# Optimization experiments

Measured on AMD Instinct MI355X. Metric: run time of the kernel, lower is better.

Reference implementation:

```python
import jax, jax.numpy as jnp
import numpy as np
from jax import lax

NEG_INF = -jnp.inf

def _conv_same(x, w, b):
    # x: [B,C,H,W], w: [O,C,5,5], padding=2 (SAME for k=5)
    y = lax.conv_general_dilated(x, w, (1, 1), [(2, 2), (2, 2)],
                                 dimension_numbers=('NCHW', 'OIHW', 'NCHW'))
    return y + b[None, :, None, None]

def _maxpool3(x):
    # kernel=3, stride=3, VALID: 28x28 -> 9x9
    return lax.reduce_window(x, -jnp.inf, lax.max, (1, 1, 3, 3), (1, 1, 3, 3), 'VALID')

def _trunk(x, w1, b1, w2, b2):
    # x: [B,1,28,28] -> [B, 16*9*9]
    h = jax.nn.relu(_conv_same(x, w1, b1))
    h = jax.nn.relu(_conv_same(h, w2, b2))
    h = _maxpool3(h)
    return h.reshape(h.shape[0], -1)

def _iterator(state, c_w1, c_b1, c_w2, c_b2, c_wl, c_bl):
    # state: [B,28,28]
    B = state.shape[0]
    xd = state[:, None]                                   # [B,1,28,28]
    feat = _trunk(xd, c_w1, c_b1, c_w2, c_b2)             # [B,1296]
    w = jnp.tanh(feat @ c_wl + c_bl).reshape(B, 1, 13, 13)  # per-sample kernels [O=B,I=1,13,13]
    xp = jnp.pad(xd, ((0, 0), (0, 0), (6, 6), (6, 6)), constant_values=-1.0)  # [B,1,40,40]
    xg = xp.reshape(1, B, 40, 40)
    yg = lax.conv_general_dilated(xg, w, (1, 1), 'VALID',
                                  feature_group_count=B,
                                  dimension_numbers=('NCHW', 'OIHW', 'NCHW'))  # [1,B,28,28]
    return yg.reshape(B, 28, 28)

def setup_inputs() -> dict:
    key = jax.random.key(0)
    ks = jax.random.split(key, 13)
    s = 0.05
    B = 1024
    inp = {
        'x': jax.random.normal(ks[0], (B, 28, 28), jnp.float32),
        # determine_n params
        'n_w1': jax.random.normal(ks[1], (8, 1, 5, 5), jnp.float32) * s,
        'n_b1': jnp.zeros((8,), jnp.float32),
        'n_w2': jax.random.normal(ks[2], (16, 8, 5, 5), jnp.float32) * s,
        'n_b2': jnp.zeros((16,), jnp.float32),
        'n_wl': jax.random.normal(ks[3], (16 * 9 * 9, 10), jnp.float32) * s,
        'n_bl': jnp.zeros((10,), jnp.float32),
        # determine_conv params
        'c_w1': jax.random.normal(ks[4], (8, 1, 5, 5), jnp.float32) * s,
        'c_b1': jnp.zeros((8,), jnp.float32),
        'c_w2': jax.random.normal(ks[5], (16, 8, 5, 5), jnp.float32) * s,
        'c_b2': jnp.zeros((16,), jnp.float32),
        'c_wl': jax.random.normal(ks[6], (16 * 9 * 9, 13 * 13), jnp.float32) * s,
        'c_bl': jnp.zeros((13 * 13,), jnp.float32),
    }
    return inp

def reference(x, n_w1, n_b1, n_w2, n_b2, n_wl, n_bl,
              c_w1, c_b1, c_w2, c_b2, c_wl, c_bl):
    B = x.shape[0]
    xd = x.reshape(B, 1, 28, 28)
    # determine_n: soft natural number over {0..9}
    num = jnp.tanh(_trunk(xd, n_w1, n_b1, n_w2, n_b2) @ n_wl + n_bl)  # [B,10]
    # TmIter: weighted sum of iterates r_0..r_9, r_{k+1} = iterator(r_k)
    r = x
    out = num[:, 0, None, None] * r
    for k in range(1, 10):  # fixed 9-step unroll (num encodes naturals 0..9)
        r = _iterator(r, c_w1, c_b1, c_w2, c_b2, c_wl, c_bl)
        out = out + num[:, k, None, None] * r
    return out.reshape(-1, 28, 28)
```

## Files before the change

kernel.cpp:

```cpp
#include <hip/hip_runtime.h>
#include <math.h>

#define RP40S 44
#define H1W   31

struct SharedBufs {
    float rp40[2][40*RP40S];
    float h1p[8*28*H1W];
    float pbuf[1296];
    float wker[13*16];
    float num_s[10];
    int   next;
};

template<int OUT, bool PAD>
__device__ __forceinline__ void fc_tanh(const float* __restrict__ Wg,
                                        const float* __restrict__ bg,
                                        const float* __restrict__ p,
                                        float* __restrict__ dst, int tid)
{
    if (tid < OUT) {
        float a[8];
        #pragma unroll
        for (int u = 0; u < 8; ++u) a[u] = 0.f;
        #pragma unroll 8
        for (int i0 = 0; i0 < 1296; i0 += 8) {
            const float4 p0 = *(const float4*)&p[i0];
            const float4 p1 = *(const float4*)&p[i0+4];
            a[0] = fmaf(p0.x, Wg[(i0+0)*OUT + tid], a[0]);
            a[1] = fmaf(p0.y, Wg[(i0+1)*OUT + tid], a[1]);
            a[2] = fmaf(p0.z, Wg[(i0+2)*OUT + tid], a[2]);
            a[3] = fmaf(p0.w, Wg[(i0+3)*OUT + tid], a[3]);
            a[4] = fmaf(p1.x, Wg[(i0+4)*OUT + tid], a[4]);
            a[5] = fmaf(p1.y, Wg[(i0+5)*OUT + tid], a[5]);
            a[6] = fmaf(p1.z, Wg[(i0+6)*OUT + tid], a[6]);
            a[7] = fmaf(p1.w, Wg[(i0+7)*OUT + tid], a[7]);
        }
        float s = ((a[0]+a[1])+(a[2]+a[3])) + ((a[4]+a[5])+(a[6]+a[7])) + bg[tid];
        dst[PAD ? (tid/13)*16 + (tid%13) : tid] = tanhf(s);
    }
}

__device__ __forceinline__ void conv1_corr(const float* __restrict__ w1g,
                                           const float* __restrict__ b1g,
                                           int c, int y,
                                           float& base, float& e0, float& e1,
                                           float& e26, float& e27)
{
    float wreg[25];
    #pragma unroll
    for (int t = 0; t < 25; ++t) wreg[t] = w1g[c*25 + t];
    float csR[5];
    float S_all = 0.f, SR = 0.f;
    #pragma unroll
    for (int kx = 0; kx < 5; ++kx) {
        float a = wreg[kx] + wreg[5+kx] + wreg[10+kx] + wreg[15+kx] + wreg[20+kx];
        float ex = 0.f;
        if (y == 0)       ex = wreg[kx] + wreg[5+kx];
        else if (y == 1)  ex = wreg[kx];
        if (y == 26)      ex += wreg[20+kx];
        else if (y == 27) ex += wreg[15+kx] + wreg[20+kx];
        csR[kx] = a - ex;
        S_all += a; SR += csR[kx];
    }
    base = b1g[c] + (S_all - SR);
    e0  = csR[0] + csR[1];
    e1  = csR[0];
    e26 = csR[4];
    e27 = csR[3] + csR[4];
}

#define C2_LOADROW(dst, YY) {                                                  \
    int rr_ = crow0 + (YY); rr_ = rr_ < 2 ? 2 : (rr_ > 29 ? 29 : rr_);         \
    const float* hp_ = plane + (rr_ - 2)*H1W;                                  \
    _Pragma("unroll") for (int j = 0; j < 13; ++j) dst[j] = hp_[j]; }

#define C2_FMAROW(src, YY)                                                     \
    if ((unsigned)(crow0 + (YY) - 2) <= 27u) {                                 \
      _Pragma("unroll") for (int t = 0; t < 3; ++t) {                          \
        const int ky_ = (YY) - t;                                              \
        if (ky_ >= 0 && ky_ <= 4) {                                            \
          _Pragma("unroll") for (int kx = 0; kx < 5; ++kx) {                   \
            const float w_ = wreg[ky_*5+kx];                                   \
            _Pragma("unroll") for (int u = 0; u < 9; ++u)                      \
              acc[t*9+u] = fmaf(w_, src[u+kx], acc[t*9+u]); } } } }

__device__ __forceinline__ void trunk_pass(SharedBufs& sb,
                                           const float* __restrict__ rpc,
                                           int tid,
                                           const float* __restrict__ w1g,
                                           const float* __restrict__ w2g,
                                           const float* __restrict__ b2g,
                                           float base, float e0, float e1,
                                           float e26, float e27)
{
    if (tid < 224) {
        const int c = tid & 7;
        const int y = tid >> 3;
        float wreg[25];
        #pragma unroll
        for (int t = 0; t < 25; ++t) wreg[t] = w1g[c*25 + t];
        float acc[28];
        #pragma unroll
        for (int x = 0; x < 28; ++x) acc[x] = base;
        acc[0]  += e0;
        acc[1]  += e1;
        acc[26] += e26;
        acc[27] += e27;
        #pragma unroll
        for (int ky = 0; ky < 5; ++ky) {
            const float4* rr = (const float4*)&rpc[(y+4+ky)*RP40S + 4];
            float rv[32];
            #pragma unroll
            for (int q = 0; q < 8; ++q) {
                float4 t = rr[q];
                rv[q*4+0]=t.x; rv[q*4+1]=t.y; rv[q*4+2]=t.z; rv[q*4+3]=t.w;
            }
            #pragma unroll
            for (int kx = 0; kx < 5; ++kx) {
                const float w = wreg[ky*5+kx];
                #pragma unroll
                for (int x = 0; x < 28; ++x) acc[x] = fmaf(w, rv[x+kx], acc[x]);
            }
        }
        float* hp = &sb.h1p[(c*28 + y)*H1W + 2];
        #pragma unroll
        for (int x = 0; x < 28; ++x) hp[x] = fmaxf(acc[x], 0.f);
    }
    __syncthreads();

    if (tid < 240) {
        const int c    = tid / 15;
        const int rem  = tid % 15;
        const int pyg  = rem / 3;
        const int pxg  = rem % 3;
        const int col0 = pxg * 9;
        const float bias = b2g[c];
        #pragma unroll 1
        for (int h = 0; h < 2; ++h) {
            const int py = pyg*2 + h;
            if (py >= 9) break;
            const int crow0 = py * 3;
            float acc[27];
            #pragma unroll
            for (int i = 0; i < 27; ++i) acc[i] = bias;
            for (int ic = 0; ic < 8; ++ic) {
                float wreg[25];
                const float* wsrc = &w2g[(c*8+ic)*25];
                #pragma unroll
                for (int t = 0; t < 25; ++t) wreg[t] = wsrc[t];
                const float* plane = &sb.h1p[ic*28*H1W + col0];
                float ra[13], rb[13];
                C2_LOADROW(ra, 0)
                C2_LOADROW(rb, 1)  C2_FMAROW(ra, 0)
                C2_LOADROW(ra, 2)  C2_FMAROW(rb, 1)
                C2_LOADROW(rb, 3)  C2_FMAROW(ra, 2)
                C2_LOADROW(ra, 4)  C2_FMAROW(rb, 3)
                C2_LOADROW(rb, 5)  C2_FMAROW(ra, 4)
                C2_LOADROW(ra, 6)  C2_FMAROW(rb, 5)
                                   C2_FMAROW(ra, 6)
            }
            #pragma unroll
            for (int pxi = 0; pxi < 3; ++pxi) {
                float m = acc[pxi*3];
                #pragma unroll
                for (int dy = 0; dy < 3; ++dy)
                    #pragma unroll
                    for (int dx = 0; dx < 3; ++dx)
                        m = fmaxf(m, acc[dy*9 + pxi*3 + dx]);
                sb.pbuf[c*81 + py*9 + pxg*3 + pxi] = fmaxf(m, 0.f);
            }
        }
    }
    __syncthreads();
}

__device__ __forceinline__ void depthwise13_regs(SharedBufs& sb,
                                                 const float* __restrict__ rpc,
                                                 int y, int x0,
                                                 float& a0, float& a1,
                                                 float& a2, float& a3)
{
    a0=0.f; a1=0.f; a2=0.f; a3=0.f;
    #pragma unroll 1
    for (int ky = 0; ky < 13; ++ky) {
        const float4* rr = (const float4*)&rpc[(y+ky)*RP40S + x0];
        float rv[16];
        #pragma unroll
        for (int q = 0; q < 4; ++q) {
            float4 t = rr[q];
            rv[q*4+0]=t.x; rv[q*4+1]=t.y; rv[q*4+2]=t.z; rv[q*4+3]=t.w;
        }
        const float4* wq = (const float4*)&sb.wker[ky*16];
        float wv[16];
        #pragma unroll
        for (int q = 0; q < 4; ++q) {
            float4 t = wq[q];
            wv[q*4+0]=t.x; wv[q*4+1]=t.y; wv[q*4+2]=t.z; wv[q*4+3]=t.w;
        }
        #pragma unroll
        for (int kx = 0; kx < 13; ++kx) {
            const float w = wv[kx];
            a0 = fmaf(w, rv[kx+0], a0);
            a1 = fmaf(w, rv[kx+1], a1);
            a2 = fmaf(w, rv[kx+2], a2);
            a3 = fmaf(w, rv[kx+3], a3);
        }
    }
}

__global__ __launch_bounds__(256) __attribute__((amdgpu_num_vgpr(168)))
void modeld_fused(const float* __restrict__ x,
                  const float* __restrict__ n_w1, const float* __restrict__ n_b1,
                  const float* __restrict__ n_w2, const float* __restrict__ n_b2,
                  const float* __restrict__ n_wl, const float* __restrict__ n_bl,
                  const float* __restrict__ c_w1, const float* __restrict__ c_b1,
                  const float* __restrict__ c_w2, const float* __restrict__ c_b2,
                  const float* __restrict__ c_wl, const float* __restrict__ c_bl,
                  float* __restrict__ out,
                  int* __restrict__ counter, int B)
{
    __shared__ SharedBufs sb;
    const int tid = threadIdx.x;
    const int dy  = tid / 7;
    const int dx0 = (tid % 7) * 4;

    float nb=0.f, ne0=0.f, ne1=0.f, ne26=0.f, ne27=0.f;
    float cb=0.f, ce0=0.f, ce1=0.f, ce26=0.f, ce27=0.f;
    if (tid < 224) {
        conv1_corr(n_w1, n_b1, tid & 7, tid >> 3, nb, ne0, ne1, ne26, ne27);
        conv1_corr(c_w1, c_b1, tid & 7, tid >> 3, cb, ce0, ce1, ce26, ce27);
    }

    for (int i = tid; i < 2*40*RP40S; i += 256) sb.rp40[0][i] = -1.f;
    for (int i = tid; i < 8*28*H1W;   i += 256) sb.h1p[i]  = 0.f;

    while (true) {
        if (tid == 0) sb.next = atomicAdd(counter, 1);
        __syncthreads();
        const int b = sb.next;
        if (b >= B) break;

        float cur[4] = {0.f, 0.f, 0.f, 0.f};
        if (tid < 196) {
            const float4 t = *(const float4*)&x[b*784 + dy*28 + dx0];
            cur[0]=t.x; cur[1]=t.y; cur[2]=t.z; cur[3]=t.w;
            float* rp = &sb.rp40[0][(dy+6)*RP40S + dx0 + 6];
            rp[0]=t.x; rp[1]=t.y; rp[2]=t.z; rp[3]=t.w;
        }
        __syncthreads();

        trunk_pass(sb, sb.rp40[0], tid, n_w1, n_w2, n_b2, nb, ne0, ne1, ne26, ne27);
        fc_tanh<10, false>(n_wl, n_bl, sb.pbuf, sb.num_s, tid);
        __syncthreads();

        float o[4];
        {
            const float n0 = sb.num_s[0];
            #pragma unroll
            for (int q = 0; q < 4; ++q) o[q] = n0 * cur[q];
        }

        int curbuf = 0;
        for (int k = 1; k <= 9; ++k) {
            const float* rpc = sb.rp40[curbuf];
            float*       rpn = sb.rp40[curbuf ^ 1];
            trunk_pass(sb, rpc, tid, c_w1, c_w2, c_b2, cb, ce0, ce1, ce26, ce27);
            fc_tanh<169, true>(c_wl, c_bl, sb.pbuf, sb.wker, tid);
            __syncthreads();
            if (tid < 196) {
                float a0, a1, a2, a3;
                depthwise13_regs(sb, rpc, dy, dx0, a0, a1, a2, a3);
                const float nk = sb.num_s[k];
                o[0] = fmaf(nk, a0, o[0]);
                o[1] = fmaf(nk, a1, o[1]);
                o[2] = fmaf(nk, a2, o[2]);
                o[3] = fmaf(nk, a3, o[3]);
                float* rp = &rpn[(dy+6)*RP40S + dx0 + 6];
                rp[0]=a0; rp[1]=a1; rp[2]=a2; rp[3]=a3;
            }
            __syncthreads();
            curbuf ^= 1;
        }

        if (tid < 196)
            *(float4*)&out[b*784 + dy*28 + dx0] = make_float4(o[0], o[1], o[2], o[3]);
    }
}

extern "C" void kernel_launch(void* const* d_in, const int* in_sizes, int n_in,
                              void* d_out, int out_size, void* d_ws, size_t ws_size,
                              hipStream_t stream)
{
    const float* x    = (const float*)d_in[0];
    const float* n_w1 = (const float*)d_in[1];
    const float* n_b1 = (const float*)d_in[2];
    const float* n_w2 = (const float*)d_in[3];
    const float* n_b2 = (const float*)d_in[4];
    const float* n_wl = (const float*)d_in[5];
    const float* n_bl = (const float*)d_in[6];
    const float* c_w1 = (const float*)d_in[7];
    const float* c_b1 = (const float*)d_in[8];
    const float* c_w2 = (const float*)d_in[9];
    const float* c_b2 = (const float*)d_in[10];
    const float* c_wl = (const float*)d_in[11];
    const float* c_bl = (const float*)d_in[12];
    float* out = (float*)d_out;

    const int B = in_sizes[0] / 784;
    hipMemsetAsync(d_ws, 0, sizeof(int), stream);
    const int grid = B < 768 ? B : 768;
    hipLaunchKernelGGL(modeld_fused, dim3(grid), dim3(256), 0, stream,
                       x, n_w1, n_b1, n_w2, n_b2, n_wl, n_bl,
                       c_w1, c_b1, c_w2, c_b2, c_wl, c_bl, out,
                       (int*)d_ws, B);
}
```

Before: 1.302 ms.

## Pre-transpose FC weights and pad conv weights in workspace for vector loads

Adds a prep kernel that transposes the 1296x169 FC weight matrix into workspace and pads the conv1 and conv2 weights to a stride of 32. Each FC thread can then stream its own contiguous row with float4 loads, and the conv weights load as float4 too. Before, each FC thread read one column with a stride of 169, which was coalesced across threads but took many scalar loads. The trade-off is an extra kernel launch and a dependence on workspace size, with a fallback path kept. Per-thread contiguous rows may coalesce worse across the wavefront than the old column reads.

```diff
diff --git a/kernel.cpp b/kernel.cpp
--- a/kernel.cpp
+++ b/kernel.cpp
@@ -3,6 +3,12 @@
 
 #define RP40S 44
 #define H1W   31
+
+#define WS_WLT    0
+#define WS_W2P    219024
+#define WS_W1P    223120
+#define WS_CNT    223376
+#define WS_FLOATS 223377
 
 struct SharedBufs {
     float rp40[2][40*RP40S];
@@ -12,6 +18,20 @@
     float num_s[10];
     int   next;
 };
+
+__global__ void prep_ws(const float* __restrict__ c_wl,
+                        const float* __restrict__ c_w2,
+                        const float* __restrict__ c_w1,
+                        float* __restrict__ ws)
+{
+    const int t = blockIdx.x*256 + threadIdx.x;
+    for (int idx = t; idx < 1296*169; idx += gridDim.x*256) {
+        const int i = idx / 169, o = idx % 169;
+        ws[WS_WLT + o*1296 + i] = c_wl[idx];
+    }
+    if (t < 128*25) ws[WS_W2P + (t/25)*32 + (t%25)] = c_w2[t];
+    if (t < 8*25)   ws[WS_W1P + (t/25)*32 + (t%25)] = c_w1[t];
+}
 
 template<int OUT, bool PAD>
 __device__ __forceinline__ void fc_tanh(const float* __restrict__ Wg,
@@ -38,6 +58,36 @@
         }
         float s = ((a[0]+a[1])+(a[2]+a[3])) + ((a[4]+a[5])+(a[6]+a[7])) + bg[tid];
         dst[PAD ? (tid/13)*16 + (tid%13) : tid] = tanhf(s);
+    }
+}
+
+__device__ __forceinline__ void fc_tanh_T169(const float* __restrict__ WT,
+                                             const float* __restrict__ bg,
+                                             const float* __restrict__ p,
+                                             float* __restrict__ dst, int tid)
+{
+    if (tid < 169) {
+        const float* wrow = WT + tid*1296;
+        float a[8];
+        #pragma unroll
+        for (int u = 0; u < 8; ++u) a[u] = 0.f;
+        #pragma unroll 8
+        for (int i0 = 0; i0 < 1296; i0 += 8) {
+            const float4 p0 = *(const float4*)&p[i0];
+            const float4 p1 = *(const float4*)&p[i0+4];
+            const float4 w0 = *(const float4*)&wrow[i0];
+            const float4 w1 = *(const float4*)&wrow[i0+4];
+            a[0] = fmaf(p0.x, w0.x, a[0]);
+            a[1] = fmaf(p0.y, w0.y, a[1]);
+            a[2] = fmaf(p0.z, w0.z, a[2]);
+            a[3] = fmaf(p0.w, w0.w, a[3]);
+            a[4] = fmaf(p1.x, w1.x, a[4]);
+            a[5] = fmaf(p1.y, w1.y, a[5]);
+            a[6] = fmaf(p1.z, w1.z, a[6]);
+            a[7] = fmaf(p1.w, w1.w, a[7]);
+        }
+        float s = ((a[0]+a[1])+(a[2]+a[3])) + ((a[4]+a[5])+(a[6]+a[7])) + bg[tid];
+        dst[(tid/13)*16 + (tid%13)] = tanhf(s);
     }
 }
 
@@ -70,6 +120,23 @@
     e27 = csR[3] + csR[4];
 }
 
+__device__ __forceinline__ void load_w25(float* wreg, const float* __restrict__ base,
+                                         bool pw)
+{
+    if (pw) {
+        const float4* q = (const float4*)base;
+        #pragma unroll
+        for (int t = 0; t < 6; ++t) {
+            float4 v = q[t];
+            wreg[4*t+0]=v.x; wreg[4*t+1]=v.y; wreg[4*t+2]=v.z; wreg[4*t+3]=v.w;
+        }
+        wreg[24] = base[24];
+    } else {
+        #pragma unroll
+        for (int t = 0; t < 25; ++t) wreg[t] = base[t];
+    }
+}
+
 #define C2_LOADROW(dst, YY) {                                                  \
     int rr_ = crow0 + (YY); rr_ = rr_ < 2 ? 2 : (rr_ > 29 ? 29 : rr_);         \
     const float* hp_ = plane + (rr_ - 2)*H1W;                                  \
@@ -91,6 +158,7 @@
                                            const float* __restrict__ w1g,
                                            const float* __restrict__ w2g,
                                            const float* __restrict__ b2g,
+                                           bool pw, int wstride,
                                            float base, float e0, float e1,
                                            float e26, float e27)
 {
@@ -98,8 +166,7 @@
         const int c = tid & 7;
         const int y = tid >> 3;
         float wreg[25];
-        #pragma unroll
-        for (int t = 0; t < 25; ++t) wreg[t] = w1g[c*25 + t];
+        load_w25(wreg, w1g + c*wstride, pw);
         float acc[28];
         #pragma unroll
         for (int x = 0; x < 28; ++x) acc[x] = base;
@@ -146,9 +213,7 @@
             for (int i = 0; i < 27; ++i) acc[i] = bias;
             for (int ic = 0; ic < 8; ++ic) {
                 float wreg[25];
-                const float* wsrc = &w2g[(c*8+ic)*25];
-                #pragma unroll
-                for (int t = 0; t < 25; ++t) wreg[t] = wsrc[t];
+                load_w25(wreg, w2g + (c*8+ic)*wstride, pw);
                 const float* plane = &sb.h1p[ic*28*H1W + col0];
                 float ra[13], rb[13];
                 C2_LOADROW(ra, 0)
@@ -218,12 +283,17 @@
                   const float* __restrict__ c_w2, const float* __restrict__ c_b2,
                   const float* __restrict__ c_wl, const float* __restrict__ c_bl,
                   float* __restrict__ out,
+                  const float* __restrict__ wsb, int use_ws,
                   int* __restrict__ counter, int B)
 {
     __shared__ SharedBufs sb;
     const int tid = threadIdx.x;
     const int dy  = tid / 7;
     const int dx0 = (tid % 7) * 4;
+
+    const float* cw1 = use_ws ? wsb + WS_W1P : c_w1;
+    const float* cw2 = use_ws ? wsb + WS_W2P : c_w2;
+    const int    cws = use_ws ? 32 : 25;
 
     float nb=0.f, ne0=0.f, ne1=0.f, ne26=0.f, ne27=0.f;
     float cb=0.f, ce0=0.f, ce1=0.f, ce26=0.f, ce27=0.f;
@@ -250,7 +320,8 @@
         }
         __syncthreads();
 
-        trunk_pass(sb, sb.rp40[0], tid, n_w1, n_w2, n_b2, nb, ne0, ne1, ne26, ne27);
+        trunk_pass(sb, sb.rp40[0], tid, n_w1, n_w2, n_b2, false, 25,
+                   nb, ne0, ne1, ne26, ne27);
         fc_tanh<10, false>(n_wl, n_bl, sb.pbuf, sb.num_s, tid);
         __syncthreads();
 
@@ -265,8 +336,10 @@
         for (int k = 1; k <= 9; ++k) {
             const float* rpc = sb.rp40[curbuf];
             float*       rpn = sb.rp40[curbuf ^ 1];
-            trunk_pass(sb, rpc, tid, c_w1, c_w2, c_b2, cb, ce0, ce1, ce26, ce27);
-            fc_tanh<169, true>(c_wl, c_bl, sb.pbuf, sb.wker, tid);
+            trunk_pass(sb, rpc, tid, cw1, cw2, c_b2, use_ws != 0, cws,
+                       cb, ce0, ce1, ce26, ce27);
+            if (use_ws) fc_tanh_T169(wsb + WS_WLT, c_bl, sb.pbuf, sb.wker, tid);
+            else        fc_tanh<169, true>(c_wl, c_bl, sb.pbuf, sb.wker, tid);
             __syncthreads();
             if (tid < 196) {
                 float a0, a1, a2, a3;
@@ -308,10 +381,18 @@
     float* out = (float*)d_out;
 
     const int B = in_sizes[0] / 784;
-    hipMemsetAsync(d_ws, 0, sizeof(int), stream);
+    const int use_ws = (ws_size >= (size_t)WS_FLOATS*4 + 4) ? 1 : 0;
+    float* wsb = (float*)d_ws;
+    int* counter = use_ws ? (int*)(wsb + WS_CNT) : (int*)d_ws;
+
+    hipMemsetAsync(counter, 0, sizeof(int), stream);
+    if (use_ws)
+        hipLaunchKernelGGL(prep_ws, dim3(512), dim3(256), 0, stream,
+                           c_wl, c_w2, c_w1, wsb);
+
     const int grid = B < 768 ? B : 768;
     hipLaunchKernelGGL(modeld_fused, dim3(grid), dim3(256), 0, stream,
                        x, n_w1, n_b1, n_w2, n_b2, n_wl, n_bl,
                        c_w1, c_b1, c_w2, c_b2, c_wl, c_bl, out,
-                       (int*)d_ws, B);
-}
+                       wsb, use_ws, counter, B);
+}
```

New measurement: 1.446 ms. 11.1% more time.
